# Performance work log

Hardware: AMD Instinct MI355X
Metric: run time of the kernel (lower is better)

The kernel has to match this reference:

```python
import jax, jax.numpy as jnp
import numpy as np

B, S, HID, CROSS = 8, 4096, 1280, 768
HEADS, HDIM = 20, 64
RANK = 128
NUM_IP, NFID_TOK, NFACE = 4, 16, 2
TEXT = 77
IP_SCALE, FID_SCALE, MID_LORA = 0.6, 0.7, 0.6
SCALE = 1.0 / (HDIM ** 0.5)


def setup_inputs() -> dict:
    key = jax.random.key(0)
    ks = iter(jax.random.split(key, 40))
    nrm = lambda sh, s=0.02: (jax.random.normal(next(ks), sh) * s).astype(jnp.float32)
    return dict(
        hidden_states=jax.random.normal(next(ks), (B, S, HID), jnp.float32),
        encoder_hidden_states=jax.random.normal(next(ks), (B, TEXT + NUM_IP + NFACE * NFID_TOK, CROSS), jnp.float32),
        wq=nrm((HID, HID)), wk=nrm((HID, CROSS)), wv=nrm((HID, CROSS)),
        wo=nrm((HID, HID)), bo=jnp.zeros((HID,), jnp.float32),
        q_ld=nrm((RANK, HID)), q_lu=nrm((HID, RANK)),
        k_ld=nrm((RANK, CROSS)), k_lu=nrm((HID, RANK)),
        v_ld=nrm((RANK, CROSS)), v_lu=nrm((HID, RANK)),
        o_ld=nrm((RANK, HID)), o_lu=nrm((HID, RANK)),
        wk_ip=nrm((HID, CROSS)), wv_ip=nrm((HID, CROSS)),
        wk_fid=nrm((HID, CROSS)), wv_fid=nrm((HID, CROSS)),
        qr_w1=nrm((HID * 2, HID)), qr_b1=jnp.zeros((HID * 2,), jnp.float32), qr_w2=nrm((HID, HID * 2)),
        kr_w1=nrm((CROSS * 2, CROSS)), kr_b1=jnp.zeros((CROSS * 2,), jnp.float32), kr_w2=nrm((HID, CROSS * 2)),
        aggr_w=nrm((1, NFID_TOK)), aggr_b=jnp.zeros((1,), jnp.float32),
    )


def _lin(x, w, b=None):
    y = x @ w.T
    return y if b is None else y + b


def reference(hidden_states, encoder_hidden_states, wq, wk, wv, wo, bo,
              q_ld, q_lu, k_ld, k_lu, v_ld, v_lu, o_ld, o_lu,
              wk_ip, wv_ip, wk_fid, wv_fid,
              qr_w1, qr_b1, qr_w2, kr_w1, kr_b1, kr_w2, aggr_w, aggr_b):
    residual = hidden_states
    Bv, Sv, _ = hidden_states.shape
    text = encoder_hidden_states[:, :TEXT]                       # prompt tokens
    ip_hs = encoder_hidden_states[:, TEXT:TEXT + NUM_IP]         # ip tokens
    fid_hs = encoder_hidden_states[:, TEXT + NUM_IP:]            # faceid tokens [B, F*T, C]

    # ---- top-1 router over faceid experts ----
    rq = _lin(jax.nn.gelu(_lin(hidden_states, qr_w1, qr_b1), approximate=False), qr_w2)  # [B,S,HID]
    r_hs = fid_hs.reshape(Bv, NFACE, NFID_TOK, CROSS)
    r_agg = jnp.einsum('bftc,t->bfc', r_hs, aggr_w[0]) + aggr_b[0]   # aggr_router over tokens
    rk = _lin(jax.nn.gelu(_lin(r_agg, kr_w1, kr_b1), approximate=False), kr_w2)          # [B,F,HID]
    logits = jnp.einsum('bsd,bfd->bsf', rq, rk)
    routing = jax.nn.one_hot(jnp.argmax(logits, axis=-1), NFACE, dtype=hidden_states.dtype)  # [B,S,F]
    routing_map = jnp.transpose(routing, (0, 2, 1))[..., None]    # [B,F,S,1]

    # ---- base QKV with multi-id LoRA (num_faceids>1 branch) ----
    query = _lin(hidden_states, wq) + MID_LORA * _lin(_lin(hidden_states, q_ld), q_lu)
    key = _lin(text, wk) + MID_LORA * _lin(_lin(text, k_ld), k_lu)
    value = _lin(text, wv) + MID_LORA * _lin(_lin(text, v_ld), v_lu)
    q = query.reshape(Bv, Sv, HEADS, HDIM)
    k = key.reshape(Bv, -1, HEADS, HDIM)
    v = value.reshape(Bv, -1, HEADS, HDIM)
    p = jax.nn.softmax(jnp.einsum('bqhd,bkhd->bhqk', q, k) * SCALE, axis=-1)
    base = jnp.einsum('bhqk,bkhd->bqhd', p, v).reshape(Bv, Sv, HID)

    # ---- IP branch ----
    ipk = _lin(ip_hs, wk_ip).reshape(Bv, -1, HEADS, HDIM)
    ipv = _lin(ip_hs, wv_ip).reshape(Bv, -1, HEADS, HDIM)
    pi = jax.nn.softmax(jnp.einsum('bqhd,bkhd->bhqk', q, ipk) * SCALE, axis=-1)
    ip_out = jnp.einsum('bhqk,bkhd->bqhd', pi, ipv).reshape(Bv, Sv, HID)

    # ---- FaceID expert branch (per-expert attention, then routed combine) ----
    fk = _lin(fid_hs, wk_fid).reshape(Bv, NFACE, NFID_TOK, HEADS, HDIM)
    fv = _lin(fid_hs, wv_fid).reshape(Bv, NFACE, NFID_TOK, HEADS, HDIM)
    pf = jax.nn.softmax(jnp.einsum('bqhd,bfthd->bfhqt', q, fk) * SCALE, axis=-1)
    f_out = jnp.einsum('bfhqt,bfthd->bfqhd', pf, fv).reshape(Bv, NFACE, Sv, HID)
    fid_out = (routing_map * f_out).sum(axis=1)                   # top-1 gather via one-hot

    h = base + IP_SCALE * ip_out + FID_SCALE * fid_out
    out = _lin(h, wo, bo) + MID_LORA * _lin(_lin(h, o_ld), o_lu)
    return out + residual
```

## Files before the change

kernel.cpp:

```cpp
#include <hip/hip_runtime.h>
#include <math.h>

#define Bc 8
#define Sc 4096
#define HIDc 1280
#define CROSSc 768
#define HEADSc 20
#define HDIMc 64
#define ETOKc 113
#define Mc (Bc * Sc)
#define CHUNKR 4096
#define NCHUNK 8
#define QRN 2560
#define QRK 3840
#define MAXFLAG 4096

typedef unsigned short u16;
typedef __attribute__((ext_vector_type(8))) short bf16x8;
typedef __attribute__((ext_vector_type(4))) float f32x4;

__device__ __forceinline__ float b2f(u16 u) {
  union { unsigned int i; float f; } x; x.i = ((unsigned int)u) << 16; return x.f;
}
__device__ __forceinline__ u16 f2b(float f) {
  union { float f; unsigned int i; } x; x.f = f;
  unsigned int r = x.i + 0x7FFFu + ((x.i >> 16) & 1u);
  return (u16)(r >> 16);
}
__device__ __forceinline__ float gelu_exact(float x) {
  return 0.5f * x * (1.0f + erff(x * 0.70710678118654752440f));
}

__device__ __forceinline__ void stage_tiles(
    const u16* __restrict__ A, int lda, int M, int r0,
    const u16* __restrict__ W, int ldw, int N, int c0,
    int k0, u16* smA, u16* smB, int wv, int lane) {
  const int srow = lane >> 3;
  const int scol = (lane & 7) * 8;
#pragma unroll
  for (int ci = 0; ci < 4; ci++) {
    int c = wv + ci * 4;
    int ar = r0 + c * 8 + srow; ar = ar < M ? ar : M - 1;
    const u16* ga = A + (size_t)ar * lda + k0 + scol;
    __builtin_amdgcn_global_load_lds((const __attribute__((address_space(1))) void*)ga,
                                     (__attribute__((address_space(3))) void*)(smA + c * 512), 16, 0, 0);
    int br = c0 + c * 8 + srow; br = br < N ? br : N - 1;
    const u16* gb = W + (size_t)br * ldw + k0 + scol;
    __builtin_amdgcn_global_load_lds((const __attribute__((address_space(1))) void*)gb,
                                     (__attribute__((address_space(3))) void*)(smB + c * 512), 16, 0, 0);
  }
}

__device__ __forceinline__ void mfma_tiles(const u16* smA, const u16* smB,
                                           int wr, int wc, int lane, f32x4 acc[4][4]) {
#pragma unroll
  for (int kh = 0; kh < 2; kh++) {
    const int ko = kh * 32 + (lane >> 4) * 8;
    bf16x8 af[4], bfv[4];
#pragma unroll
    for (int i = 0; i < 4; i++)
      af[i] = *(const bf16x8*)(smA + (wr * 64 + i * 16 + (lane & 15)) * 64 + ko);
#pragma unroll
    for (int j = 0; j < 4; j++)
      bfv[j] = *(const bf16x8*)(smB + (wc * 64 + j * 16 + (lane & 15)) * 64 + ko);
#pragma unroll
    for (int i = 0; i < 4; i++)
#pragma unroll
      for (int j = 0; j < 4; j++)
        acc[i][j] = __builtin_amdgcn_mfma_f32_16x16x32_bf16(af[i], bfv[j], acc[i][j], 0, 0, 0);
  }
}

template <int CMODE>
__global__ __launch_bounds__(256) void gemm_bf16(
    const u16* __restrict__ A, int lda, const u16* __restrict__ W, int ldw,
    int M, int N, int K, float alpha, const float* __restrict__ bias,
    const void* __restrict__ addp, void* __restrict__ Cp) {
  __shared__ __align__(16) u16 smA[128 * 64];
  __shared__ __align__(16) u16 smB[128 * 64];
  const int t = threadIdx.x, lane = t & 63, wv = t >> 6;
  const int wr = wv >> 1, wc = wv & 1;
  const int r0 = blockIdx.y * 128, c0 = blockIdx.x * 128;
  f32x4 acc[4][4] = {};
  for (int k0 = 0; k0 < K; k0 += 64) {
    stage_tiles(A, lda, M, r0, W, ldw, N, c0, k0, smA, smB, wv, lane);
    __syncthreads();
    mfma_tiles(smA, smB, wr, wc, lane, acc);
    __syncthreads();
  }
  const int cl = lane & 15, quad = lane >> 4;
#pragma unroll
  for (int i = 0; i < 4; i++) {
#pragma unroll
    for (int j = 0; j < 4; j++) {
      int gc = c0 + wc * 64 + j * 16 + cl;
      if (gc >= N) continue;
      float bv = bias ? bias[gc] : 0.0f;
#pragma unroll
      for (int r = 0; r < 4; r++) {
        int gr = r0 + wr * 64 + i * 16 + quad * 4 + r;
        if (gr >= M) continue;
        float v = alpha * acc[i][j][r] + bv;
        if (CMODE == 0) {
          const float* add = (const float*)addp;
          if (add) v += add[(size_t)gr * N + gc];
          ((float*)Cp)[(size_t)gr * N + gc] = v;
        } else {
          const u16* add = (const u16*)addp;
          if (add) v += b2f(add[(size_t)gr * N + gc]);
          ((u16*)Cp)[(size_t)gr * N + gc] = f2b(v);
        }
      }
    }
  }
}

__global__ __launch_bounds__(256) void gemm_qr(
    const u16* __restrict__ A, const u16* __restrict__ W,
    const float* __restrict__ b1, const float* __restrict__ crk0,
    const float* __restrict__ crk1, float* __restrict__ LOG, int mbase) {
  __shared__ __align__(16) u16 smA[128 * 64];
  __shared__ __align__(16) u16 smB[128 * 64];
  const int t = threadIdx.x, lane = t & 63, wv = t >> 6;
  const int wr = wv >> 1, wc = wv & 1;
  const int r0 = blockIdx.y * 128, c0 = blockIdx.x * 128;
  f32x4 acc[4][4] = {};
  for (int k0 = 0; k0 < QRK; k0 += 64) {
    stage_tiles(A, QRK, CHUNKR, r0, W, QRK, QRN, c0, k0, smA, smB, wv, lane);
    __syncthreads();
    mfma_tiles(smA, smB, wr, wc, lane, acc);
    __syncthreads();
  }
  const int cl = lane & 15, quad = lane >> 4;
#pragma unroll
  for (int i = 0; i < 4; i++) {
    float p0[4] = {0.f, 0.f, 0.f, 0.f};
    float p1[4] = {0.f, 0.f, 0.f, 0.f};
#pragma unroll
    for (int j = 0; j < 4; j++) {
      int gc = c0 + wc * 64 + j * 16 + cl;
      float bv = b1[gc], c0v = crk0[gc], c1v = crk1[gc];
#pragma unroll
      for (int r = 0; r < 4; r++) {
        float g = gelu_exact(acc[i][j][r] + bv);
        p0[r] = fmaf(g, c0v, p0[r]);
        p1[r] = fmaf(g, c1v, p1[r]);
      }
    }
#pragma unroll
    for (int off = 1; off < 16; off <<= 1) {
#pragma unroll
      for (int r = 0; r < 4; r++) {
        p0[r] += __shfl_xor(p0[r], off);
        p1[r] += __shfl_xor(p1[r], off);
      }
    }
    if (cl == 0) {
#pragma unroll
      for (int r = 0; r < 4; r++) {
        int gm = mbase + r0 + wr * 64 + i * 16 + quad * 4 + r;
        atomicAdd(&LOG[2 * gm + 0], p0[r]);
        atomicAdd(&LOG[2 * gm + 1], p1[r]);
      }
    }
  }
}

__global__ void cast_bf16_kernel(const float* __restrict__ src, u16* __restrict__ dst, int n4) {
  int i = blockIdx.x * 256 + threadIdx.x;
  if (i >= n4) return;
  float4 v = ((const float4*)src)[i];
  ushort4 o;
  o.x = f2b(v.x); o.y = f2b(v.y); o.z = f2b(v.z); o.w = f2b(v.w);
  ((ushort4*)dst)[i] = o;
}

__global__ void castX_chunk_kernel(const float* __restrict__ X, u16* __restrict__ Xb,
                                   u16* __restrict__ Xcat, int rowstart) {
  int i = blockIdx.x * 256 + threadIdx.x;
  if (i >= CHUNKR * HIDc) return;
  int r = i / HIDc, c = i % HIDc;
  float x = X[(size_t)(rowstart + r) * HIDc + c];
  u16 hi = f2b(x);
  u16 lob = f2b(x - b2f(hi));
  Xb[(size_t)(rowstart + r) * HIDc + c] = hi;
  size_t rb = (size_t)r * QRK;
  Xcat[rb + c] = hi; Xcat[rb + HIDc + c] = hi; Xcat[rb + 2 * HIDc + c] = lob;
}

__global__ void cast_w1_kernel(const float* __restrict__ w1, u16* __restrict__ W1cat) {
  int i = blockIdx.x * 256 + threadIdx.x;
  if (i >= QRN * HIDc) return;
  int r = i / HIDc, c = i % HIDc;
  float w = w1[i];
  u16 hi = f2b(w);
  u16 lob = f2b(w - b2f(hi));
  size_t rb = (size_t)r * QRK;
  W1cat[rb + c] = hi; W1cat[rb + HIDc + c] = lob; W1cat[rb + 2 * HIDc + c] = hi;
}

__global__ void slice_kernel(const float* __restrict__ E, u16* __restrict__ txt,
                             u16* __restrict__ ip, u16* __restrict__ fid) {
  int i = blockIdx.x * 256 + threadIdx.x;
  if (i >= Bc * ETOKc * CROSSc) return;
  int c = i % CROSSc;
  int rr = i / CROSSc;
  int tok = rr % ETOKc, b = rr / ETOKc;
  u16 v = f2b(E[i]);
  if (tok < 77) txt[((size_t)b * 77 + tok) * CROSSc + c] = v;
  else if (tok < 81) ip[((size_t)b * 4 + (tok - 77)) * CROSSc + c] = v;
  else fid[((size_t)b * 32 + (tok - 81)) * CROSSc + c] = v;
}

__global__ void ragg_kernel(const float* __restrict__ E, const float* __restrict__ aw,
                            const float* __restrict__ ab, float* __restrict__ ragg) {
  int i = blockIdx.x * 256 + threadIdx.x;
  if (i >= Bc * 2 * CROSSc) return;
  int c = i % CROSSc;
  int f = (i / CROSSc) & 1;
  int b = i / (2 * CROSSc);
  const float* base = E + ((size_t)b * ETOKc + 81 + f * 16) * CROSSc + c;
  float s = ab[0];
#pragma unroll
  for (int tk = 0; tk < 16; tk++) s = fmaf(base[tk * CROSSc], aw[tk], s);
  ragg[i] = s;
}

__global__ void kr1_kernel(const float* __restrict__ ragg, const float* __restrict__ w1,
                           const float* __restrict__ b1, float* __restrict__ kr1) {
  int i = blockIdx.x * 256 + threadIdx.x;
  if (i >= 16 * 1536) return;
  int j = i % 1536, bf = i / 1536;
  const float* a = ragg + (size_t)bf * CROSSc;
  const float* w = w1 + (size_t)j * CROSSc;
  float s = b1[j];
  for (int c = 0; c < CROSSc; c++) s = fmaf(a[c], w[c], s);
  kr1[i] = gelu_exact(s);
}

__global__ void rk_kernel(const float* __restrict__ kr1, const float* __restrict__ w2,
                          float* __restrict__ rk) {
  int i = blockIdx.x * 256 + threadIdx.x;
  if (i >= 16 * HIDc) return;
  int d = i % HIDc, bf = i / HIDc;
  const float* a = kr1 + (size_t)bf * 1536;
  const float* w = w2 + (size_t)d * 1536;
  float s = 0.f;
  for (int j = 0; j < 1536; j++) s = fmaf(a[j], w[j], s);
  rk[i] = s;
}

__global__ void crk_kernel(const float* __restrict__ rk, const float* __restrict__ qr_w2,
                           float* __restrict__ crk) {
  int i = blockIdx.x * 256 + threadIdx.x;
  if (i >= 16 * QRN) return;
  int e = i % QRN, bf = i / QRN;
  const float* r = rk + (size_t)bf * HIDc;
  float s = 0.f;
  for (int d = 0; d < HIDc; d++) s = fmaf(r[d], qr_w2[(size_t)d * QRN + e], s);
  crk[i] = s;
}

__global__ void tau_kernel(const float* __restrict__ crk, float* __restrict__ tau) {
  __shared__ float red[256];
  int t = threadIdx.x, b = blockIdx.x;
  const float* c0 = crk + (size_t)(b * 2) * QRN;
  const float* c1 = c0 + QRN;
  float s = 0.f;
  for (int e = t; e < QRN; e += 256) { float d = c0[e] - c1[e]; s = fmaf(d, d, s); }
  red[t] = s; __syncthreads();
  for (int o = 128; o; o >>= 1) { if (t < o) red[t] += red[t + o]; __syncthreads(); }
  if (t == 0) tau[b] = 1e-4f * sqrtf(red[0]);
}

__global__ void route_flag_kernel(const float* __restrict__ LOG, const float* __restrict__ tau,
                                  int* __restrict__ route, int* __restrict__ flags,
                                  int* __restrict__ count) {
  int i = blockIdx.x * 256 + threadIdx.x;
  if (i >= Mc) return;
  float l0 = LOG[2 * i], l1 = LOG[2 * i + 1];
  route[i] = (l1 > l0) ? 1 : 0;
  if (fabsf(l1 - l0) < tau[i >> 12]) {
    int idx = atomicAdd(count, 1);
    if (idx < MAXFLAG) flags[idx] = i;
  }
}

__global__ __launch_bounds__(256) void fixup_kernel(
    const float* __restrict__ X, const float* __restrict__ w1,
    const float* __restrict__ b1, const float* __restrict__ crk,
    const int* __restrict__ flags, const int* __restrict__ count,
    int* __restrict__ route) {
  __shared__ float xr[HIDc];
  __shared__ float r0s[4], r1s[4];
  int n = *count; if (n > MAXFLAG) n = MAXFLAG;
  for (int fi = blockIdx.x; fi < n; fi += gridDim.x) {
    int m = flags[fi];
    int b = m >> 12;
    __syncthreads();
    for (int k = threadIdx.x; k < HIDc; k += 256) xr[k] = X[(size_t)m * HIDc + k];
    __syncthreads();
    float p0 = 0.f, p1 = 0.f;
    for (int e = threadIdx.x; e < QRN; e += 256) {
      const float* w = w1 + (size_t)e * HIDc;
      float s = b1[e];
      for (int k = 0; k < HIDc; k++) s = fmaf(xr[k], w[k], s);
      float g = gelu_exact(s);
      p0 = fmaf(g, crk[(size_t)(b * 2) * QRN + e], p0);
      p1 = fmaf(g, crk[(size_t)(b * 2 + 1) * QRN + e], p1);
    }
    for (int o = 32; o; o >>= 1) { p0 += __shfl_down(p0, o); p1 += __shfl_down(p1, o); }
    int wvi = threadIdx.x >> 6;
    if ((threadIdx.x & 63) == 0) { r0s[wvi] = p0; r1s[wvi] = p1; }
    __syncthreads();
    if (threadIdx.x == 0)
      route[m] = ((r1s[0] + r1s[1] + r1s[2] + r1s[3]) >
                  (r0s[0] + r0s[1] + r0s[2] + r0s[3])) ? 1 : 0;
    __syncthreads();
  }
}

__global__ __launch_bounds__(256) void attn_kernel(
    const u16* __restrict__ Q, const float* __restrict__ Kb,
    const float* __restrict__ Vb, const float* __restrict__ IPK,
    const float* __restrict__ IPV, const float* __restrict__ FK,
    const float* __restrict__ FV, const int* __restrict__ route,
    u16* __restrict__ H) {
  __shared__ __align__(16) u16 K_lds[128 * 64];
  __shared__ __align__(16) u16 V_t[64 * 136];
  __shared__ __align__(16) u16 P_lds[4 * 32 * 136];
  const int t = threadIdx.x, lane = t & 63, wv = t >> 6;
  const int cl = lane & 15, quad = lane >> 4, qr4 = quad * 4;
  const int b = blockIdx.z, hh = blockIdx.y;
  const int s0 = blockIdx.x * 128;

  for (int idx = t; idx < 128 * 16; idx += 256) {
    const int row = idx >> 4, c4 = idx & 15;
    float4 v = make_float4(0.f, 0.f, 0.f, 0.f);
    const float* src = nullptr;
    if (row < 77)                    src = Kb  + ((size_t)(b * 77 + row)) * HIDc;
    else if (row >= 80 && row < 84)  src = IPK + ((size_t)(b * 4 + row - 80)) * HIDc;
    else if (row >= 96)              src = FK  + ((size_t)(b * 32 + row - 96)) * HIDc;
    if (src) v = ((const float4*)(src + hh * HDIMc))[c4];
    unsigned int w0 = ((unsigned int)f2b(v.y) << 16) | f2b(v.x);
    unsigned int w1 = ((unsigned int)f2b(v.w) << 16) | f2b(v.z);
    int byte = (row * 128 + c4 * 8) ^ ((row & 7) << 4);
    *(uint2*)((char*)K_lds + byte) = make_uint2(w0, w1);
  }
  for (int idx = t; idx < 128 * 16; idx += 256) {
    const int row = idx >> 4, c4 = idx & 15;
    float4 v = make_float4(0.f, 0.f, 0.f, 0.f);
    const float* src = nullptr;
    if (row < 77)                    src = Vb  + ((size_t)(b * 77 + row)) * HIDc;
    else if (row >= 80 && row < 84)  src = IPV + ((size_t)(b * 4 + row - 80)) * HIDc;
    else if (row >= 96)              src = FV  + ((size_t)(b * 32 + row - 96)) * HIDc;
    if (src) v = ((const float4*)(src + hh * HDIMc))[c4];
    V_t[(c4 * 4 + 0) * 136 + row] = f2b(v.x);
    V_t[(c4 * 4 + 1) * 136 + row] = f2b(v.y);
    V_t[(c4 * 4 + 2) * 136 + row] = f2b(v.z);
    V_t[(c4 * 4 + 3) * 136 + row] = f2b(v.w);
  }
  __syncthreads();

  const size_t mbase = (size_t)b * Sc + s0 + wv * 32;
  bf16x8 qf[2][2];
#pragma unroll
  for (int ni = 0; ni < 2; ni++)
#pragma unroll
    for (int kk = 0; kk < 2; kk++)
      qf[ni][kk] = *(const bf16x8*)(Q + (mbase + ni * 16 + cl) * HIDc + hh * HDIMc + kk * 32 + quad * 8);
  const int face[2] = { route[mbase + cl], route[mbase + 16 + cl] };

  f32x4 acc[8][2] = {};
#pragma unroll
  for (int kk = 0; kk < 2; kk++) {
    bf16x8 af[8];
#pragma unroll
    for (int mi = 0; mi < 8; mi++) {
      const int row = mi * 16 + cl;
      const int byte = (row * 128 + (kk * 32 + quad * 8) * 2) ^ ((row & 7) << 4);
      af[mi] = *(const bf16x8*)((const char*)K_lds + byte);
    }
#pragma unroll
    for (int mi = 0; mi < 8; mi++)
#pragma unroll
      for (int ni = 0; ni < 2; ni++)
        acc[mi][ni] = __builtin_amdgcn_mfma_f32_16x16x32_bf16(af[mi], qf[ni][kk], acc[mi][ni], 0, 0, 0);
  }

  u16* Pw = P_lds + wv * 32 * 136;
  const float NEG = -1e30f;
#pragma unroll
  for (int ni = 0; ni < 2; ni++) {
    float e[8][4];
#pragma unroll
    for (int mi = 0; mi < 8; mi++)
#pragma unroll
      for (int r = 0; r < 4; r++) e[mi][r] = 0.125f * acc[mi][ni][r];
#pragma unroll
    for (int r = 0; r < 4; r++) {
      e[4][r] = (qr4 + r <= 12) ? e[4][r] : NEG;
      e[5][r] = (quad == 0) ? e[5][r] : NEG;
    }
    float mt = NEG;
#pragma unroll
    for (int mi = 0; mi < 5; mi++)
#pragma unroll
      for (int r = 0; r < 4; r++) mt = fmaxf(mt, e[mi][r]);
    mt = fmaxf(mt, __shfl_xor(mt, 16));
    mt = fmaxf(mt, __shfl_xor(mt, 32));
    float lt = 0.f;
#pragma unroll
    for (int mi = 0; mi < 5; mi++)
#pragma unroll
      for (int r = 0; r < 4; r++) { e[mi][r] = __expf(e[mi][r] - mt); lt += e[mi][r]; }
    lt += __shfl_xor(lt, 16); lt += __shfl_xor(lt, 32);
    float mp = NEG;
#pragma unroll
    for (int r = 0; r < 4; r++) mp = fmaxf(mp, e[5][r]);
    mp = fmaxf(mp, __shfl_xor(mp, 16));
    mp = fmaxf(mp, __shfl_xor(mp, 32));
    float lp = 0.f;
#pragma unroll
    for (int r = 0; r < 4; r++) { e[5][r] = __expf(e[5][r] - mp); lp += e[5][r]; }
    lp += __shfl_xor(lp, 16); lp += __shfl_xor(lp, 32);
    const int f = face[ni];
    float sf[4];
#pragma unroll
    for (int r = 0; r < 4; r++) sf[r] = f ? e[7][r] : e[6][r];
    float mf = NEG;
#pragma unroll
    for (int r = 0; r < 4; r++) mf = fmaxf(mf, sf[r]);
    mf = fmaxf(mf, __shfl_xor(mf, 16));
    mf = fmaxf(mf, __shfl_xor(mf, 32));
    float lf = 0.f;
#pragma unroll
    for (int r = 0; r < 4; r++) { sf[r] = __expf(sf[r] - mf); lf += sf[r]; }
    lf += __shfl_xor(lf, 16); lf += __shfl_xor(lf, 32);
    const float sct = 1.0f / lt, sci = 0.6f / lp, scf = 0.7f / lf;
#pragma unroll
    for (int mi = 0; mi < 5; mi++)
#pragma unroll
      for (int r = 0; r < 4; r++) e[mi][r] *= sct;
#pragma unroll
    for (int r = 0; r < 4; r++) {
      e[5][r] *= sci;
      const float pf = sf[r] * scf;
      e[6][r] = f ? 0.f : pf;
      e[7][r] = f ? pf : 0.f;
    }
    u16* prow = Pw + (ni * 16 + cl) * 136 + qr4;
#pragma unroll
    for (int mi = 0; mi < 8; mi++) {
      unsigned int a0 = (unsigned int)f2b(e[mi][0]) | ((unsigned int)f2b(e[mi][1]) << 16);
      unsigned int a1 = (unsigned int)f2b(e[mi][2]) | ((unsigned int)f2b(e[mi][3]) << 16);
      *(uint2*)(prow + mi * 16) = make_uint2(a0, a1);
    }
  }

  f32x4 pacc[2][4] = {};
#pragma unroll
  for (int kk = 0; kk < 4; kk++) {
    bf16x8 pa[2], vb[4];
#pragma unroll
    for (int mi2 = 0; mi2 < 2; mi2++)
      pa[mi2] = *(const bf16x8*)(Pw + (mi2 * 16 + cl) * 136 + kk * 32 + quad * 8);
#pragma unroll
    for (int ni2 = 0; ni2 < 4; ni2++)
      vb[ni2] = *(const bf16x8*)(V_t + (ni2 * 16 + cl) * 136 + kk * 32 + quad * 8);
#pragma unroll
    for (int mi2 = 0; mi2 < 2; mi2++)
#pragma unroll
      for (int ni2 = 0; ni2 < 4; ni2++)
        pacc[mi2][ni2] = __builtin_amdgcn_mfma_f32_16x16x32_bf16(pa[mi2], vb[ni2], pacc[mi2][ni2], 0, 0, 0);
  }
#pragma unroll
  for (int mi2 = 0; mi2 < 2; mi2++) {
#pragma unroll
    for (int r = 0; r < 4; r++) {
      u16* hp = H + (mbase + mi2 * 16 + qr4 + r) * HIDc + hh * HDIMc + cl;
#pragma unroll
      for (int ni2 = 0; ni2 < 4; ni2++)
        hp[ni2 * 16] = f2b(pacc[mi2][ni2][r]);
    }
  }
}

extern "C" void kernel_launch(void* const* d_in, const int* in_sizes, int n_in,
                              void* d_out, int out_size, void* d_ws, size_t ws_size,
                              hipStream_t stream) {
  (void)in_sizes; (void)n_in; (void)out_size; (void)ws_size;
  const float* X      = (const float*)d_in[0];
  const float* E      = (const float*)d_in[1];
  const float* wq     = (const float*)d_in[2];
  const float* wk     = (const float*)d_in[3];
  const float* wv     = (const float*)d_in[4];
  const float* wo     = (const float*)d_in[5];
  const float* bo     = (const float*)d_in[6];
  const float* q_ld   = (const float*)d_in[7];
  const float* q_lu   = (const float*)d_in[8];
  const float* k_ld   = (const float*)d_in[9];
  const float* k_lu   = (const float*)d_in[10];
  const float* v_ld   = (const float*)d_in[11];
  const float* v_lu   = (const float*)d_in[12];
  const float* o_ld   = (const float*)d_in[13];
  const float* o_lu   = (const float*)d_in[14];
  const float* wk_ip  = (const float*)d_in[15];
  const float* wv_ip  = (const float*)d_in[16];
  const float* wk_fid = (const float*)d_in[17];
  const float* wv_fid = (const float*)d_in[18];
  const float* qr_w1  = (const float*)d_in[19];
  const float* qr_b1  = (const float*)d_in[20];
  const float* qr_w2  = (const float*)d_in[21];
  const float* kr_w1  = (const float*)d_in[22];
  const float* kr_b1  = (const float*)d_in[23];
  const float* kr_w2  = (const float*)d_in[24];
  const float* aggr_w = (const float*)d_in[25];
  const float* aggr_b = (const float*)d_in[26];
  float* out = (float*)d_out;

  char* base = (char*)d_ws;
  size_t off = 0;
  auto alloc = [&](size_t bytes) -> void* {
    off = (off + 255) & ~(size_t)255;
    void* p = base + off; off += bytes; return p;
  };
  u16* Xb    = (u16*)alloc((size_t)Mc * HIDc * 2);
  u16* Xcat  = (u16*)alloc((size_t)CHUNKR * QRK * 2);
  u16* W1cat = (u16*)alloc((size_t)QRN * QRK * 2);
  u16* Qb    = (u16*)alloc((size_t)Mc * HIDc * 2);
  u16* Hb    = (u16*)alloc((size_t)Mc * HIDc * 2);
  u16* TMPb  = (u16*)alloc((size_t)Mc * 128 * 2);
  u16* TMPo  = (u16*)alloc((size_t)Mc * 128 * 2);
  float* Kb  = (float*)alloc((size_t)Bc * 77 * HIDc * 4);
  float* Vb  = (float*)alloc((size_t)Bc * 77 * HIDc * 4);
  float* IPK = (float*)alloc((size_t)Bc * 4 * HIDc * 4);
  float* IPV = (float*)alloc((size_t)Bc * 4 * HIDc * 4);
  float* FK  = (float*)alloc((size_t)Bc * 32 * HIDc * 4);
  float* FV  = (float*)alloc((size_t)Bc * 32 * HIDc * 4);
  u16* TXTb  = (u16*)alloc((size_t)Bc * 77 * CROSSc * 2);
  u16* IPCb  = (u16*)alloc((size_t)Bc * 4 * CROSSc * 2);
  u16* FIDCb = (u16*)alloc((size_t)Bc * 32 * CROSSc * 2);
  u16* TTb   = (u16*)alloc((size_t)Bc * 77 * 128 * 2);
  u16* wqb   = (u16*)alloc((size_t)HIDc * HIDc * 2);
  u16* wob   = (u16*)alloc((size_t)HIDc * HIDc * 2);
  u16* wkb   = (u16*)alloc((size_t)HIDc * CROSSc * 2);
  u16* wvb   = (u16*)alloc((size_t)HIDc * CROSSc * 2);
  u16* wkipb = (u16*)alloc((size_t)HIDc * CROSSc * 2);
  u16* wvipb = (u16*)alloc((size_t)HIDc * CROSSc * 2);
  u16* wkfb  = (u16*)alloc((size_t)HIDc * CROSSc * 2);
  u16* wvfb  = (u16*)alloc((size_t)HIDc * CROSSc * 2);
  u16* qldb  = (u16*)alloc((size_t)128 * HIDc * 2);
  u16* qlub  = (u16*)alloc((size_t)HIDc * 128 * 2);
  u16* kldb  = (u16*)alloc((size_t)128 * CROSSc * 2);
  u16* klub  = (u16*)alloc((size_t)HIDc * 128 * 2);
  u16* vldb  = (u16*)alloc((size_t)128 * CROSSc * 2);
  u16* vlub  = (u16*)alloc((size_t)HIDc * 128 * 2);
  u16* oldb  = (u16*)alloc((size_t)128 * HIDc * 2);
  u16* olub  = (u16*)alloc((size_t)HIDc * 128 * 2);
  float* RAGG = (float*)alloc(16 * CROSSc * 4);
  float* KR1  = (float*)alloc(16 * 1536 * 4);
  float* RK   = (float*)alloc(16 * HIDc * 4);
  float* CRK  = (float*)alloc(16 * QRN * 4);
  float* TAU  = (float*)alloc(Bc * 4);
  float* LOG  = (float*)alloc((size_t)Mc * 2 * 4);
  int* ROUTE  = (int*)alloc((size_t)Mc * 4);
  int* FLAGS  = (int*)alloc(MAXFLAG * 4);
  int* COUNT  = (int*)alloc(4);

  auto castW = [&](const float* s, u16* d, int n) {
    cast_bf16_kernel<<<(n / 4 + 255) / 256, 256, 0, stream>>>(s, d, n / 4);
  };
  auto G0 = [&](const u16* A, int lda, const u16* W, int ldw, int M, int N, int K,
                float alpha, const float* bias, const float* add, float* C) {
    gemm_bf16<0><<<dim3(N / 128, (M + 127) / 128), 256, 0, stream>>>(
        A, lda, W, ldw, M, N, K, alpha, bias, (const void*)add, (void*)C);
  };
  auto G1 = [&](const u16* A, int lda, const u16* W, int ldw, int M, int N, int K,
                float alpha, const u16* add, u16* C) {
    gemm_bf16<1><<<dim3(N / 128, (M + 127) / 128), 256, 0, stream>>>(
        A, lda, W, ldw, M, N, K, alpha, nullptr, (const void*)add, (void*)C);
  };

  slice_kernel<<<(Bc * ETOKc * CROSSc + 255) / 256, 256, 0, stream>>>(E, TXTb, IPCb, FIDCb);
  ragg_kernel<<<(Bc * 2 * CROSSc + 255) / 256, 256, 0, stream>>>(E, aggr_w, aggr_b, RAGG);
  kr1_kernel<<<(16 * 1536 + 255) / 256, 256, 0, stream>>>(RAGG, kr_w1, kr_b1, KR1);
  rk_kernel<<<(16 * HIDc + 255) / 256, 256, 0, stream>>>(KR1, kr_w2, RK);
  crk_kernel<<<(16 * QRN + 255) / 256, 256, 0, stream>>>(RK, qr_w2, CRK);
  tau_kernel<<<Bc, 256, 0, stream>>>(CRK, TAU);

  castW(wq, wqb, HIDc * HIDc);     castW(wo, wob, HIDc * HIDc);
  castW(wk, wkb, HIDc * CROSSc);   castW(wv, wvb, HIDc * CROSSc);
  castW(wk_ip, wkipb, HIDc * CROSSc); castW(wv_ip, wvipb, HIDc * CROSSc);
  castW(wk_fid, wkfb, HIDc * CROSSc); castW(wv_fid, wvfb, HIDc * CROSSc);
  castW(q_ld, qldb, 128 * HIDc);   castW(q_lu, qlub, HIDc * 128);
  castW(k_ld, kldb, 128 * CROSSc); castW(k_lu, klub, HIDc * 128);
  castW(v_ld, vldb, 128 * CROSSc); castW(v_lu, vlub, HIDc * 128);
  castW(o_ld, oldb, 128 * HIDc);   castW(o_lu, olub, HIDc * 128);
  cast_w1_kernel<<<(QRN * HIDc + 255) / 256, 256, 0, stream>>>(qr_w1, W1cat);

  hipMemsetAsync(LOG, 0, (size_t)Mc * 2 * 4, stream);
  hipMemsetAsync(COUNT, 0, 4, stream);
  for (int ch = 0; ch < NCHUNK; ch++) {
    castX_chunk_kernel<<<(CHUNKR * HIDc + 255) / 256, 256, 0, stream>>>(X, Xb, Xcat, ch * CHUNKR);
    gemm_qr<<<dim3(QRN / 128, CHUNKR / 128), 256, 0, stream>>>(
        Xcat, W1cat, qr_b1, CRK + (size_t)(ch * 2) * QRN, CRK + (size_t)(ch * 2 + 1) * QRN,
        LOG, ch * CHUNKR);
  }
  route_flag_kernel<<<(Mc + 255) / 256, 256, 0, stream>>>(LOG, TAU, ROUTE, FLAGS, COUNT);
  fixup_kernel<<<64, 256, 0, stream>>>(X, qr_w1, qr_b1, CRK, FLAGS, COUNT, ROUTE);

  G1(Xb, HIDc, qldb, HIDc, Mc, 128, HIDc, 1.0f, nullptr, TMPb);
  G1(Xb, HIDc, wqb, HIDc, Mc, HIDc, HIDc, 1.0f, nullptr, Qb);
  G1(TMPb, 128, qlub, 128, Mc, HIDc, 128, 0.6f, Qb, Qb);

  const int Mt = Bc * 77;
  G0(TXTb, CROSSc, wkb, CROSSc, Mt, HIDc, CROSSc, 1.0f, nullptr, nullptr, Kb);
  G1(TXTb, CROSSc, kldb, CROSSc, Mt, 128, CROSSc, 1.0f, nullptr, TTb);
  G0(TTb, 128, klub, 128, Mt, HIDc, 128, 0.6f, nullptr, Kb, Kb);
  G0(TXTb, CROSSc, wvb, CROSSc, Mt, HIDc, CROSSc, 1.0f, nullptr, nullptr, Vb);
  G1(TXTb, CROSSc, vldb, CROSSc, Mt, 128, CROSSc, 1.0f, nullptr, TTb);
  G0(TTb, 128, vlub, 128, Mt, HIDc, 128, 0.6f, nullptr, Vb, Vb);

  G0(IPCb, CROSSc, wkipb, CROSSc, Bc * 4, HIDc, CROSSc, 1.0f, nullptr, nullptr, IPK);
  G0(IPCb, CROSSc, wvipb, CROSSc, Bc * 4, HIDc, CROSSc, 1.0f, nullptr, nullptr, IPV);
  G0(FIDCb, CROSSc, wkfb, CROSSc, Bc * 32, HIDc, CROSSc, 1.0f, nullptr, nullptr, FK);
  G0(FIDCb, CROSSc, wvfb, CROSSc, Bc * 32, HIDc, CROSSc, 1.0f, nullptr, nullptr, FV);

  attn_kernel<<<dim3(Sc / 128, HEADSc, Bc), 256, 0, stream>>>(Qb, Kb, Vb, IPK, IPV, FK, FV, ROUTE, Hb);

  G1(Hb, HIDc, oldb, HIDc, Mc, 128, HIDc, 1.0f, nullptr, TMPo);
  G0(TMPo, 128, olub, 128, Mc, HIDc, 128, 0.6f, bo, X, out);
  G0(Hb, HIDc, wob, HIDc, Mc, HIDc, HIDc, 1.0f, nullptr, out, out);
}
```

Measured before the change: 4.272 ms.

## Split router fixup across expert slices with coalesced wave-level dot products

```diff
diff --git a/kernel.cpp b/kernel.cpp
--- a/kernel.cpp
+++ b/kernel.cpp
@@ -14,6 +14,8 @@
 #define QRN 2560
 #define QRK 3840
 #define MAXFLAG 4096
+#define NSLICE 32
+#define ESLICE (QRN / NSLICE)
 
 typedef unsigned short u16;
 typedef __attribute__((ext_vector_type(8))) short bf16x8;
@@ -286,38 +288,49 @@
   }
 }
 
-__global__ __launch_bounds__(256) void fixup_kernel(
+__global__ __launch_bounds__(256) void fixup_partial(
     const float* __restrict__ X, const float* __restrict__ w1,
     const float* __restrict__ b1, const float* __restrict__ crk,
     const int* __restrict__ flags, const int* __restrict__ count,
-    int* __restrict__ route) {
+    float* __restrict__ fixp) {
   __shared__ float xr[HIDc];
-  __shared__ float r0s[4], r1s[4];
   int n = *count; if (n > MAXFLAG) n = MAXFLAG;
-  for (int fi = blockIdx.x; fi < n; fi += gridDim.x) {
-    int m = flags[fi];
-    int b = m >> 12;
+  const int t = threadIdx.x, lane = t & 63, wv = t >> 6;
+  for (int w = blockIdx.x; w < n * NSLICE; w += gridDim.x) {
+    const int fi = w / NSLICE, sl = w % NSLICE;
+    const int m = flags[fi], b = m >> 12;
     __syncthreads();
-    for (int k = threadIdx.x; k < HIDc; k += 256) xr[k] = X[(size_t)m * HIDc + k];
+    for (int k = t; k < HIDc; k += 256) xr[k] = X[(size_t)m * HIDc + k];
     __syncthreads();
     float p0 = 0.f, p1 = 0.f;
-    for (int e = threadIdx.x; e < QRN; e += 256) {
-      const float* w = w1 + (size_t)e * HIDc;
-      float s = b1[e];
-      for (int k = 0; k < HIDc; k++) s = fmaf(xr[k], w[k], s);
-      float g = gelu_exact(s);
-      p0 = fmaf(g, crk[(size_t)(b * 2) * QRN + e], p0);
-      p1 = fmaf(g, crk[(size_t)(b * 2 + 1) * QRN + e], p1);
-    }
-    for (int o = 32; o; o >>= 1) { p0 += __shfl_down(p0, o); p1 += __shfl_down(p1, o); }
-    int wvi = threadIdx.x >> 6;
-    if ((threadIdx.x & 63) == 0) { r0s[wvi] = p0; r1s[wvi] = p1; }
-    __syncthreads();
-    if (threadIdx.x == 0)
-      route[m] = ((r1s[0] + r1s[1] + r1s[2] + r1s[3]) >
-                  (r0s[0] + r0s[1] + r0s[2] + r0s[3])) ? 1 : 0;
-    __syncthreads();
-  }
+    const int ebase = sl * ESLICE + wv * (ESLICE / 4);
+#pragma unroll 4
+    for (int j = 0; j < ESLICE / 4; j++) {
+      const int e = ebase + j;
+      const float* wrow = w1 + (size_t)e * HIDc;
+      float s = 0.f;
+      for (int k = lane; k < HIDc; k += 64) s = fmaf(xr[k], wrow[k], s);
+#pragma unroll
+      for (int o = 1; o < 64; o <<= 1) s += __shfl_xor(s, o);
+      if (lane == 0) {
+        float g = gelu_exact(s + b1[e]);
+        p0 = fmaf(g, crk[(size_t)(b * 2) * QRN + e], p0);
+        p1 = fmaf(g, crk[(size_t)(b * 2 + 1) * QRN + e], p1);
+      }
+    }
+    if (lane == 0) {
+      atomicAdd(&fixp[2 * fi + 0], p0);
+      atomicAdd(&fixp[2 * fi + 1], p1);
+    }
+  }
+}
+
+__global__ void fixup_final(const float* __restrict__ fixp, const int* __restrict__ flags,
+                            const int* __restrict__ count, int* __restrict__ route) {
+  int n = *count; if (n > MAXFLAG) n = MAXFLAG;
+  int i = blockIdx.x * 256 + threadIdx.x;
+  if (i >= n) return;
+  route[flags[i]] = (fixp[2 * i + 1] > fixp[2 * i]) ? 1 : 0;
 }
 
 __global__ __launch_bounds__(256) void attn_kernel(
@@ -567,6 +580,7 @@
   int* ROUTE  = (int*)alloc((size_t)Mc * 4);
   int* FLAGS  = (int*)alloc(MAXFLAG * 4);
   int* COUNT  = (int*)alloc(4);
+  float* FIXP = (float*)alloc((size_t)MAXFLAG * 2 * 4);
 
   auto castW = [&](const float* s, u16* d, int n) {
     cast_bf16_kernel<<<(n / 4 + 255) / 256, 256, 0, stream>>>(s, d, n / 4);
@@ -601,6 +615,7 @@
 
   hipMemsetAsync(LOG, 0, (size_t)Mc * 2 * 4, stream);
   hipMemsetAsync(COUNT, 0, 4, stream);
+  hipMemsetAsync(FIXP, 0, (size_t)MAXFLAG * 2 * 4, stream);
   for (int ch = 0; ch < NCHUNK; ch++) {
     castX_chunk_kernel<<<(CHUNKR * HIDc + 255) / 256, 256, 0, stream>>>(X, Xb, Xcat, ch * CHUNKR);
     gemm_qr<<<dim3(QRN / 128, CHUNKR / 128), 256, 0, stream>>>(
@@ -608,7 +623,8 @@
         LOG, ch * CHUNKR);
   }
   route_flag_kernel<<<(Mc + 255) / 256, 256, 0, stream>>>(LOG, TAU, ROUTE, FLAGS, COUNT);
-  fixup_kernel<<<64, 256, 0, stream>>>(X, qr_w1, qr_b1, CRK, FLAGS, COUNT, ROUTE);
+  fixup_partial<<<2048, 256, 0, stream>>>(X, qr_w1, qr_b1, CRK, FLAGS, COUNT, FIXP);
+  fixup_final<<<MAXFLAG / 256, 256, 0, stream>>>(FIXP, FLAGS, COUNT, ROUTE);
 
   G1(Xb, HIDc, qldb, HIDc, Mc, 128, HIDc, 1.0f, nullptr, TMPb);
   G1(Xb, HIDc, wqb, HIDc, Mc, HIDc, HIDc, 1.0f, nullptr, Qb);
```

After: 3.924 ms. 1.09x faster.
